# Kernel optimization log

Hardware: AMD Instinct MI355X
Metric: run time of the kernel (lower is better)

Reference implementation:

```python
import jax, jax.numpy as jnp
import numpy as np
from jax import lax

XI = 2.0
RADIUS = int(3 * XI)  # 6 -> kernel size 13


def _gaussian_weight(xi: float):
    radius = int(3 * xi)
    coords = jnp.arange(-radius, radius + 1, dtype=jnp.float32)
    g1 = jnp.exp(-coords ** 2 / (2.0 * xi * xi))
    g1 = g1 / g1.sum()
    g3 = g1[:, None, None] * g1[None, :, None] * g1[None, None, :]  # (K,K,K)
    # grouped conv weight: (out_ch=3, in_ch/groups=1, K, K, K), same kernel per channel
    return jnp.broadcast_to(g3[None, None], (3, 1) + g3.shape)


def setup_inputs() -> dict:
    key = jax.random.key(0)
    x = jax.random.normal(key, (1, 3, 192, 192, 192), dtype=jnp.float32)
    w = _gaussian_weight(XI)
    return {"x": x, "w": w}


def reference(x, w):
    # depthwise (groups=3) 3D cross-correlation with 'same' padding = radius,
    # matching nn.Conv3d(3, 3, (K,K,K), padding=radius, groups=3, bias=False)
    r = (w.shape[-1] - 1) // 2
    return lax.conv_general_dilated(
        x, w,
        window_strides=(1, 1, 1),
        padding=[(r, r)] * 3,
        dimension_numbers=("NCDHW", "OIDHW", "NCDHW"),
        feature_group_count=3,
    )
```

## Files before the change

### kernel.cpp

```cpp
#include <hip/hip_runtime.h>

#define RAD 6
#define KS 13
#define DIM 192
#define CH 3
#define W4C 48
#define PLANE4 (DIM * W4C)
#define VOL4 (DIM * PLANE4)
#define VOL (DIM * DIM * DIM)
#define TOTAL (CH * VOL)

__global__ void g1_extract_kernel(const float* __restrict__ w, float* __restrict__ g1) {
    int i = threadIdx.x;
    if (i < KS) {
        float s = 0.f;
        for (int j = 0; j < KS * KS; ++j) s += w[i * KS * KS + j];
        g1[i] = s;
    }
}

#define HT 32
#define HL 48
#define NT1 192
#define NLD (HL * W4C)

__global__ __launch_bounds__(NT1) void conv_wh2(const float* __restrict__ in,
                                                float* __restrict__ out,
                                                const float* __restrict__ g1) {
    __shared__ float4 tile[NLD];
    const int bid = blockIdx.x;
    const int ht = bid % 6;
    const int d = (bid / 6) % DIM;
    const int c = bid / (6 * DIM);
    const int h0 = ht * HT;
    const int t = threadIdx.x;

    float g[KS];
#pragma unroll
    for (int k = 0; k < KS; ++k) g[k] = g1[k];

    const float4* in4 = (const float4*)in;
    float4* out4 = (float4*)out;
    const size_t plane = (size_t)c * VOL4 + (size_t)d * PLANE4;
    const float4 z4 = make_float4(0.f, 0.f, 0.f, 0.f);

#pragma unroll
    for (int i = 0; i < 12; ++i) {
        int idx = t + i * NT1;
        int row = idx / W4C, w4 = idx % W4C;
        int h = h0 - 8 + row;
        int hc = min(max(h, 0), DIM - 1);
        float4 v = in4[plane + (size_t)hc * W4C + w4];
        if (h < 0 || h >= DIM) v = z4;
        tile[idx] = v;
    }
    __syncthreads();

    float4 va[12];
#pragma unroll
    for (int i = 0; i < 12; ++i) {
        int idx = t + i * NT1;
        int row = idx / W4C, w4 = idx % W4C;
        int w0 = w4 * 4;
        float f[20];
#pragma unroll
        for (int b = 0; b < 5; ++b) {
            int j = min(max(w4 + b - 2, 0), W4C - 1);
            float4 v = tile[row * W4C + j];
            f[4 * b + 0] = v.x; f[4 * b + 1] = v.y;
            f[4 * b + 2] = v.z; f[4 * b + 3] = v.w;
        }
#pragma unroll
        for (int j = 0; j < 20; ++j) {
            int ww = w0 - 8 + j;
            if (ww < 0 || ww >= DIM) f[j] = 0.f;
        }
        float4 o = z4;
#pragma unroll
        for (int k = 0; k < KS; ++k) {
            o.x += g[k] * f[k + 2];
            o.y += g[k] * f[k + 3];
            o.z += g[k] * f[k + 4];
            o.w += g[k] * f[k + 5];
        }
        va[i] = o;
    }
    __syncthreads();
#pragma unroll
    for (int i = 0; i < 12; ++i) tile[t + i * NT1] = va[i];
    __syncthreads();

    const int w4 = t % W4C;
    const int rg = t / W4C;
    const int i0 = rg * 8;
    float4 buf[KS];
#pragma unroll
    for (int j = 0; j < KS; ++j) buf[j] = tile[(i0 + 2 + j) * W4C + w4];

#pragma unroll
    for (int ii = 0; ii < 8; ++ii) {
        float4 a = z4;
#pragma unroll
        for (int j = 0; j < KS; ++j) {
            const float4 v = buf[(ii + j) % KS];
            float gw = g[j];
            a.x += gw * v.x; a.y += gw * v.y; a.z += gw * v.z; a.w += gw * v.w;
        }
        out4[plane + (size_t)(h0 + i0 + ii) * W4C + w4] = a;
        if (ii < 7) buf[ii % KS] = tile[(i0 + ii + 15) * W4C + w4];
    }
}

__global__ __launch_bounds__(256) void conv_d8(const float* __restrict__ in,
                                               float* __restrict__ out,
                                               const float* __restrict__ g1) {
    __shared__ float4 tile[DIM * 8];
    const int bid = blockIdx.x;
    const int wt = bid % 6;
    const int h = (bid / 6) % DIM;
    const int c = bid / (6 * DIM);
    const int t = threadIdx.x;

    float g[KS];
#pragma unroll
    for (int k = 0; k < KS; ++k) g[k] = g1[k];

    const float4* in4 = (const float4*)in;
    float4* out4 = (float4*)out;
    const size_t base4 = (size_t)c * VOL4 + (size_t)h * W4C + wt * 8;
    const float4 z4 = make_float4(0.f, 0.f, 0.f, 0.f);

#pragma unroll
    for (int i = 0; i < 6; ++i) {
        int idx = t + i * 256;
        int dd = idx / 8, w = idx % 8;
        tile[idx] = in4[base4 + (size_t)dd * PLANE4 + w];
    }
    __syncthreads();

    const int w = t % 8;
    const int seg = t / 8;
    const int d0 = seg * 6;

    float4 buf[KS];
#pragma unroll
    for (int j = 0; j < KS; ++j) {
        int p = d0 - RAD + j;
        buf[j] = (p >= 0 && p < DIM) ? tile[p * 8 + w] : z4;
    }

#pragma unroll
    for (int i = 0; i < 6; ++i) {
        float4 a = z4;
#pragma unroll
        for (int j = 0; j < KS; ++j) {
            const float4 v = buf[(i + j) % KS];
            float gw = g[j];
            a.x += gw * v.x; a.y += gw * v.y; a.z += gw * v.z; a.w += gw * v.w;
        }
        out4[base4 + (size_t)(d0 + i) * PLANE4 + w] = a;
        if (i < 5) {
            int p = d0 + i + RAD + 1;
            buf[i % KS] = (p < DIM) ? tile[p * 8 + w] : z4;
        }
    }
}

__global__ void naive_conv3d_kernel(const float* __restrict__ x, const float* __restrict__ w,
                                    float* __restrict__ out, int total) {
    int n = blockIdx.x * blockDim.x + threadIdx.x;
    if (n >= total) return;
    int wp = n % DIM;
    int h = (n / DIM) % DIM;
    int d = (n / (DIM * DIM)) % DIM;
    int c = n / (DIM * DIM * DIM);
    const float* wc = w + c * KS * KS * KS;
    const float* xc = x + (size_t)c * DIM * DIM * DIM;
    float acc = 0.f;
    for (int kd = 0; kd < KS; ++kd) {
        int dd = d + kd - RAD;
        if (dd < 0 || dd >= DIM) continue;
        for (int kh = 0; kh < KS; ++kh) {
            int hh = h + kh - RAD;
            if (hh < 0 || hh >= DIM) continue;
            for (int kw = 0; kw < KS; ++kw) {
                int ww = wp + kw - RAD;
                if (ww < 0 || ww >= DIM) continue;
                acc += wc[(kd * KS + kh) * KS + kw] * xc[((size_t)dd * DIM + hh) * DIM + ww];
            }
        }
    }
    out[n] = acc;
}

extern "C" void kernel_launch(void* const* d_in, const int* in_sizes, int n_in,
                              void* d_out, int out_size, void* d_ws, size_t ws_size,
                              hipStream_t stream) {
    const float* x = (const float*)d_in[0];
    const float* w = (const float*)d_in[1];
    float* out = (float*)d_out;

    const size_t inter_bytes = (size_t)TOTAL * sizeof(float);

    if (ws_size >= inter_bytes + 64) {
        float* inter = (float*)d_ws;
        float* g1 = (float*)((char*)d_ws + inter_bytes);

        g1_extract_kernel<<<1, 64, 0, stream>>>(w, g1);

        conv_wh2<<<CH * DIM * 6, NT1, 0, stream>>>(x, inter, g1);

        conv_d8<<<CH * DIM * 6, 256, 0, stream>>>(inter, out, g1);
    } else {
        const int threads = 256;
        const int blocks = (TOTAL + threads - 1) / threads;
        naive_conv3d_kernel<<<blocks, threads, 0, stream>>>(x, w, out, TOTAL);
    }
}
```

Before: 191.2 us.

## Fuse separable W/H/D passes into one kernel with register sliding window over depth

Replaces the two-kernel pipeline (W+H pass to a global intermediate, then a D pass) with a single kernel. Each block owns an 8-row H tile and a 12-plane D tile, streams input planes through LDS to do the W and H passes, and keeps the last 13 plane results in registers for the D pass. This removes the full-volume intermediate write and reread, and the block index is swizzled so neighbouring blocks land on different XCDs. In exchange it recomputes a 12-plane depth halo for every 12 output planes (about twice the W/H work), puts two barriers on each plane step, and uses many registers. It also uses nontemporal stores.

```diff
diff --git a/kernel.cpp b/kernel.cpp
--- a/kernel.cpp
+++ b/kernel.cpp
@@ -10,6 +10,19 @@
 #define VOL (DIM * DIM * DIM)
 #define TOTAL (CH * VOL)
 
+#define HT 8
+#define HL 20
+#define DT 12
+#define NDT 16
+#define NSTEP (DT + 2 * RAD)
+#define NTF 192
+#define NHT (DIM / HT)
+#define GRIDF (CH * NHT * NDT)
+#define RS 49
+#define WCS 49
+
+typedef float nt4 __attribute__((ext_vector_type(4)));
+
 __global__ void g1_extract_kernel(const float* __restrict__ w, float* __restrict__ g1) {
     int i = threadIdx.x;
     if (i < KS) {
@@ -19,150 +32,133 @@
     }
 }
 
-#define HT 32
-#define HL 48
-#define NT1 192
-#define NLD (HL * W4C)
-
-__global__ __launch_bounds__(NT1) void conv_wh2(const float* __restrict__ in,
-                                                float* __restrict__ out,
-                                                const float* __restrict__ g1) {
-    __shared__ float4 tile[NLD];
-    const int bid = blockIdx.x;
-    const int ht = bid % 6;
-    const int d = (bid / 6) % DIM;
-    const int c = bid / (6 * DIM);
+__global__ __launch_bounds__(NTF) void conv3d_fused(const float* __restrict__ in,
+                                                    float* __restrict__ out,
+                                                    const float* __restrict__ g1v) {
+    __shared__ float4 raw[HL * RS];
+    __shared__ float4 wcb[HL * WCS];
+
+    int bid = blockIdx.x;
+    bid = (bid & 7) * (GRIDF / 8) + (bid >> 3);
+    const int ht = bid % NHT;
+    const int dt = (bid / NHT) % NDT;
+    const int c  = bid / (NHT * NDT);
     const int h0 = ht * HT;
-    const int t = threadIdx.x;
+    const int d0 = dt * DT;
+    const int t  = threadIdx.x;
 
     float g[KS];
 #pragma unroll
-    for (int k = 0; k < KS; ++k) g[k] = g1[k];
-
-    const float4* in4 = (const float4*)in;
-    float4* out4 = (float4*)out;
-    const size_t plane = (size_t)c * VOL4 + (size_t)d * PLANE4;
+    for (int k = 0; k < KS; ++k) g[k] = g1v[k];
+
+    const float4* __restrict__ in4 = (const float4*)in;
+    float4* __restrict__ out4 = (float4*)out;
     const float4 z4 = make_float4(0.f, 0.f, 0.f, 0.f);
 
-#pragma unroll
-    for (int i = 0; i < 12; ++i) {
-        int idx = t + i * NT1;
-        int row = idx / W4C, w4 = idx % W4C;
-        int h = h0 - 8 + row;
+    const int w4 = t % W4C;
+    const int pj = t / W4C;
+
+    int srcOff[5];
+#pragma unroll
+    for (int i = 0; i < 5; ++i) {
+        int r = pj + 4 * i;
+        int h = h0 - RAD + r;
         int hc = min(max(h, 0), DIM - 1);
-        float4 v = in4[plane + (size_t)hc * W4C + w4];
-        if (h < 0 || h >= DIM) v = z4;
-        tile[idx] = v;
-    }
-    __syncthreads();
-
-    float4 va[12];
-#pragma unroll
-    for (int i = 0; i < 12; ++i) {
-        int idx = t + i * NT1;
-        int row = idx / W4C, w4 = idx % W4C;
-        int w0 = w4 * 4;
-        float f[20];
-#pragma unroll
-        for (int b = 0; b < 5; ++b) {
-            int j = min(max(w4 + b - 2, 0), W4C - 1);
-            float4 v = tile[row * W4C + j];
-            f[4 * b + 0] = v.x; f[4 * b + 1] = v.y;
-            f[4 * b + 2] = v.z; f[4 * b + 3] = v.w;
+        srcOff[i] = c * VOL4 + hc * W4C + w4;
+    }
+
+    const int u_run = t >> 3;
+    const int seg = t & 7;
+    const bool runActive = (t < HL * 8);
+    const int hrow = h0 - RAD + u_run;
+    const float rowScale = (hrow >= 0 && hrow < DIM) ? 1.f : 0.f;
+    const bool segLo = (seg == 0);
+    const bool segHi = (seg == 7);
+    const int rawRow = u_run * RS;
+    const int wcBase = u_run * WCS + seg * 6;
+
+    const int tapBase = 2 * pj * WCS + w4;
+    const int outBase = c * VOL4 + (h0 + 2 * pj) * W4C + w4;
+
+    float4 WA[14], WB[14];
+#pragma unroll
+    for (int j = 0; j < 14; ++j) { WA[j] = z4; WB[j] = z4; }
+
+#pragma unroll 1
+    for (int s2 = 0; s2 < NSTEP; s2 += 2) {
+#pragma unroll
+        for (int off = 0; off < 2; ++off) {
+            const int s = s2 + off;
+            const int dp = d0 - RAD + s;
+            const bool dpv = (dp >= 0) && (dp < DIM);
+            float4 whA = z4, whB = z4;
+            if (dpv) {
+                const int pb = dp * PLANE4;
+#pragma unroll
+                for (int i = 0; i < 5; ++i) {
+                    float4 v = in4[pb + srcOff[i]];
+                    raw[(pj + 4 * i) * RS + w4] = v;
+                }
+                __syncthreads();
+                if (runActive) {
+                    float F[40];
+#pragma unroll
+                    for (int i = 0; i < 10; ++i) {
+                        int cw = seg * 6 - 2 + i;
+                        int cwc = min(max(cw, 0), W4C - 1);
+                        float4 v = raw[rawRow + cwc];
+                        if ((segLo && i < 2) || (segHi && i >= 8)) v = z4;
+                        F[4*i+0] = v.x; F[4*i+1] = v.y;
+                        F[4*i+2] = v.z; F[4*i+3] = v.w;
+                    }
+#pragma unroll
+                    for (int q = 0; q < 6; ++q) {
+                        float ax = 0.f, ay = 0.f, az = 0.f, aw = 0.f;
+#pragma unroll
+                        for (int k = 0; k < KS; ++k) {
+                            const float gw = g[k];
+                            ax += gw * F[4*q + 2 + k];
+                            ay += gw * F[4*q + 3 + k];
+                            az += gw * F[4*q + 4 + k];
+                            aw += gw * F[4*q + 5 + k];
+                        }
+                        wcb[wcBase + q] = make_float4(ax * rowScale, ay * rowScale,
+                                                      az * rowScale, aw * rowScale);
+                    }
+                }
+                __syncthreads();
+                float4 T[14];
+#pragma unroll
+                for (int k = 0; k < 14; ++k) T[k] = wcb[tapBase + k * WCS];
+#pragma unroll
+                for (int k = 0; k < KS; ++k) {
+                    const float gw = g[k];
+                    whA.x += gw * T[k].x;   whA.y += gw * T[k].y;
+                    whA.z += gw * T[k].z;   whA.w += gw * T[k].w;
+                    whB.x += gw * T[k+1].x; whB.y += gw * T[k+1].y;
+                    whB.z += gw * T[k+1].z; whB.w += gw * T[k+1].w;
+                }
+            }
+            if (off == 0) { WA[12] = whA; WB[12] = whB; }
+            else          { WA[13] = whA; WB[13] = whB; }
+            if (s2 >= 2 * RAD) {
+                const int o = d0 + s - 2 * RAD;
+                float4 A = z4, B = z4;
+#pragma unroll
+                for (int j = 0; j < KS; ++j) {
+                    const float gw = g[j];
+                    const float4 a = WA[j + off];
+                    const float4 b = WB[j + off];
+                    A.x += gw * a.x; A.y += gw * a.y; A.z += gw * a.z; A.w += gw * a.w;
+                    B.x += gw * b.x; B.y += gw * b.y; B.z += gw * b.z; B.w += gw * b.w;
+                }
+                const int ob = outBase + o * PLANE4;
+                __builtin_nontemporal_store(*(const nt4*)&A, (nt4*)&out4[ob]);
+                __builtin_nontemporal_store(*(const nt4*)&B, (nt4*)&out4[ob + W4C]);
+            }
         }
 #pragma unroll
-        for (int j = 0; j < 20; ++j) {
-            int ww = w0 - 8 + j;
-            if (ww < 0 || ww >= DIM) f[j] = 0.f;
-        }
-        float4 o = z4;
-#pragma unroll
-        for (int k = 0; k < KS; ++k) {
-            o.x += g[k] * f[k + 2];
-            o.y += g[k] * f[k + 3];
-            o.z += g[k] * f[k + 4];
-            o.w += g[k] * f[k + 5];
-        }
-        va[i] = o;
-    }
-    __syncthreads();
-#pragma unroll
-    for (int i = 0; i < 12; ++i) tile[t + i * NT1] = va[i];
-    __syncthreads();
-
-    const int w4 = t % W4C;
-    const int rg = t / W4C;
-    const int i0 = rg * 8;
-    float4 buf[KS];
-#pragma unroll
-    for (int j = 0; j < KS; ++j) buf[j] = tile[(i0 + 2 + j) * W4C + w4];
-
-#pragma unroll
-    for (int ii = 0; ii < 8; ++ii) {
-        float4 a = z4;
-#pragma unroll
-        for (int j = 0; j < KS; ++j) {
-            const float4 v = buf[(ii + j) % KS];
-            float gw = g[j];
-            a.x += gw * v.x; a.y += gw * v.y; a.z += gw * v.z; a.w += gw * v.w;
-        }
-        out4[plane + (size_t)(h0 + i0 + ii) * W4C + w4] = a;
-        if (ii < 7) buf[ii % KS] = tile[(i0 + ii + 15) * W4C + w4];
-    }
-}
-
-__global__ __launch_bounds__(256) void conv_d8(const float* __restrict__ in,
-                                               float* __restrict__ out,
-                                               const float* __restrict__ g1) {
-    __shared__ float4 tile[DIM * 8];
-    const int bid = blockIdx.x;
-    const int wt = bid % 6;
-    const int h = (bid / 6) % DIM;
-    const int c = bid / (6 * DIM);
-    const int t = threadIdx.x;
-
-    float g[KS];
-#pragma unroll
-    for (int k = 0; k < KS; ++k) g[k] = g1[k];
-
-    const float4* in4 = (const float4*)in;
-    float4* out4 = (float4*)out;
-    const size_t base4 = (size_t)c * VOL4 + (size_t)h * W4C + wt * 8;
-    const float4 z4 = make_float4(0.f, 0.f, 0.f, 0.f);
-
-#pragma unroll
-    for (int i = 0; i < 6; ++i) {
-        int idx = t + i * 256;
-        int dd = idx / 8, w = idx % 8;
-        tile[idx] = in4[base4 + (size_t)dd * PLANE4 + w];
-    }
-    __syncthreads();
-
-    const int w = t % 8;
-    const int seg = t / 8;
-    const int d0 = seg * 6;
-
-    float4 buf[KS];
-#pragma unroll
-    for (int j = 0; j < KS; ++j) {
-        int p = d0 - RAD + j;
-        buf[j] = (p >= 0 && p < DIM) ? tile[p * 8 + w] : z4;
-    }
-
-#pragma unroll
-    for (int i = 0; i < 6; ++i) {
-        float4 a = z4;
-#pragma unroll
-        for (int j = 0; j < KS; ++j) {
-            const float4 v = buf[(i + j) % KS];
-            float gw = g[j];
-            a.x += gw * v.x; a.y += gw * v.y; a.z += gw * v.z; a.w += gw * v.w;
-        }
-        out4[base4 + (size_t)(d0 + i) * PLANE4 + w] = a;
-        if (i < 5) {
-            int p = d0 + i + RAD + 1;
-            buf[i % KS] = (p < DIM) ? tile[p * 8 + w] : z4;
-        }
+        for (int j = 0; j < 12; ++j) { WA[j] = WA[j + 2]; WB[j] = WB[j + 2]; }
     }
 }
 
@@ -200,17 +196,10 @@
     const float* w = (const float*)d_in[1];
     float* out = (float*)d_out;
 
-    const size_t inter_bytes = (size_t)TOTAL * sizeof(float);
-
-    if (ws_size >= inter_bytes + 64) {
-        float* inter = (float*)d_ws;
-        float* g1 = (float*)((char*)d_ws + inter_bytes);
-
+    if (ws_size >= 64) {
+        float* g1 = (float*)d_ws;
         g1_extract_kernel<<<1, 64, 0, stream>>>(w, g1);
-
-        conv_wh2<<<CH * DIM * 6, NT1, 0, stream>>>(x, inter, g1);
-
-        conv_d8<<<CH * DIM * 6, 256, 0, stream>>>(inter, out, g1);
+        conv3d_fused<<<GRIDF, NTF, 0, stream>>>(x, out, g1);
     } else {
         const int threads = 256;
         const int blocks = (TOTAL + threads - 1) / threads;
```

Measured after the change: 240.2 us. +25.6%, slower.
